# Kernel optimization log

Hardware: AMD Instinct MI355X
Metric: run time of the kernel (lower is better)

## Reference

```python
import jax, jax.numpy as jnp
import numpy as np

B, T, D, H, N = 16, 512, 256, 4, 10
DK = D // H
EPS = 1e-12  # espnet LayerNorm eps


def _pe(t, d):
    # espnet PositionalEncoding table
    pos = np.arange(t, dtype=np.float32)[:, None]
    div = np.exp(np.arange(0, d, 2, dtype=np.float32) * (-np.log(10000.0) / d))
    pe = np.zeros((t, d), dtype=np.float32)
    pe[:, 0::2] = np.sin(pos * div)
    pe[:, 1::2] = np.cos(pos * div)
    return jnp.asarray(pe)


def _ln(x, g, b):
    m = jnp.mean(x, -1, keepdims=True)
    v = jnp.var(x, -1, keepdims=True)
    return (x - m) * jax.lax.rsqrt(v + EPS) * g + b


def _forward(x, x_lengths, lids, Wq, bq, Wk, bk, Wv, bv, Wo, bo, W1, b1, W2, b2, g1, be1, g2, be2, gf, bef):
    b, t, d = x.shape
    pe = _pe(t, d)
    pad = jnp.arange(t)[None, :] < x_lengths[:, None]          # [b,t] non-pad mask
    amask = pad[:, None, None, :]                               # [b,1,1,t] key mask
    onehot = (lids[:, None] == jnp.arange(N)[None, :]).astype(x.dtype)  # [b,N]
    h0 = x * np.float32(np.sqrt(d)) + pe[None]                  # scaled input + pos-enc (shared across experts)
    neg = jnp.finfo(x.dtype).min
    out = jnp.zeros_like(x)
    for z in range(N):  # fixed small set of structurally-distinct experts
        # pre-norm self-attention block
        hn = _ln(h0, g1[z], be1[z])
        q = (hn @ Wq[z] + bq[z]).reshape(b, t, H, DK).transpose(0, 2, 1, 3)
        k_ = (hn @ Wk[z] + bk[z]).reshape(b, t, H, DK).transpose(0, 2, 1, 3)
        v_ = (hn @ Wv[z] + bv[z]).reshape(b, t, H, DK).transpose(0, 2, 1, 3)
        scores = jnp.einsum('bhqd,bhkd->bhqk', q, k_) / np.float32(np.sqrt(DK))
        attn = jax.nn.softmax(jnp.where(amask, scores, neg), axis=-1)
        attn = jnp.where(amask, attn, jnp.zeros((), x.dtype))
        ctx = jnp.einsum('bhqk,bhkd->bhqd', attn, v_).transpose(0, 2, 1, 3).reshape(b, t, d)
        h = h0 + ctx @ Wo[z] + bo[z]
        # pre-norm feed-forward block
        hn2 = _ln(h, g2[z], be2[z])
        h = h + jax.nn.relu(hn2 @ W1[z] + b1[z]) @ W2[z] + b2[z]
        # final after_norm, then one-hot masked combine (== emb_lang sum)
        out = out + onehot[:, z, None, None] * _ln(h, gf[z], bef[z])
    return out


def setup_inputs() -> dict:
    key = jax.random.key(0)
    ks = jax.random.split(key, 12)
    s = np.float32(0.02)
    FF = 4 * D
    return {
        'x': jax.random.normal(ks[0], (B, T, D), jnp.float32),
        'x_lengths': jax.random.randint(ks[1], (B,), T // 2, T + 1),
        'lids': jax.random.randint(ks[2], (B,), 0, N),
        'Wq': jax.random.normal(ks[3], (N, D, D), jnp.float32) * s,
        'bq': jnp.zeros((N, D), jnp.float32),
        'Wk': jax.random.normal(ks[4], (N, D, D), jnp.float32) * s,
        'bk': jnp.zeros((N, D), jnp.float32),
        'Wv': jax.random.normal(ks[5], (N, D, D), jnp.float32) * s,
        'bv': jnp.zeros((N, D), jnp.float32),
        'Wo': jax.random.normal(ks[6], (N, D, D), jnp.float32) * s,
        'bo': jnp.zeros((N, D), jnp.float32),
        'W1': jax.random.normal(ks[7], (N, D, FF), jnp.float32) * s,
        'b1': jnp.zeros((N, FF), jnp.float32),
        'W2': jax.random.normal(ks[8], (N, FF, D), jnp.float32) * s,
        'b2': jnp.zeros((N, D), jnp.float32),
        'g1': jnp.ones((N, D), jnp.float32),
        'be1': jnp.zeros((N, D), jnp.float32),
        'g2': jnp.ones((N, D), jnp.float32),
        'be2': jnp.zeros((N, D), jnp.float32),
        'gf': jnp.ones((N, D), jnp.float32),
        'bef': jnp.zeros((N, D), jnp.float32),
    }


def reference(x, x_lengths, lids, Wq, bq, Wk, bk, Wv, bv, Wo, bo, W1, b1, W2, b2, g1, be1, g2, be2, gf, bef):
    return _forward(x, x_lengths, lids, Wq, bq, Wk, bk, Wv, bv, Wo, bo, W1, b1, W2, b2, g1, be1, g2, be2, gf, bef)
```

## Files before the change

kernel.cpp:

```cpp
#include <hip/hip_runtime.h>

typedef unsigned short u16;
typedef __bf16 bf16x8 __attribute__((ext_vector_type(8)));
typedef float  f32x4  __attribute__((ext_vector_type(4)));
typedef unsigned int   u32x4 __attribute__((ext_vector_type(4)));
typedef unsigned short u16x4 __attribute__((ext_vector_type(4)));

#define DEV __device__ __forceinline__

#define NB   16
#define TT   512
#define DD   256
#define HH   4
#define DKH  64
#define NLANG 10
#define FFD  1024

DEV u16 f2bf(float f) {
  unsigned int u = __builtin_bit_cast(unsigned int, f);
  return (u16)((u + 0x7fffu + ((u >> 16) & 1u)) >> 16);
}

DEV f32x4 zero4() { f32x4 z; z[0]=0.f; z[1]=0.f; z[2]=0.f; z[3]=0.f; return z; }

typedef __attribute__((address_space(1))) const unsigned int g_as1;
typedef __attribute__((address_space(3))) unsigned int l_as3;
DEV void load_lds16(const void* g, void* l) {
  __builtin_amdgcn_global_load_lds((g_as1*)g, (l_as3*)l, 16, 0, 0);
}

DEV bf16x8 lds_frag(const u16* lds, int row, int slot) {
  return *(const bf16x8*)(lds + row * 64 + ((slot ^ (row & 7)) << 3));
}

__global__ __launch_bounds__(256) void pre_kernel(
    const float* __restrict__ Wq, const float* __restrict__ Wk,
    const float* __restrict__ Wv, const float* __restrict__ Wo,
    const float* __restrict__ W1, const float* __restrict__ W2,
    u16* __restrict__ wtq, u16* __restrict__ wtk, u16* __restrict__ wtv,
    u16* __restrict__ wto, u16* __restrict__ wt1, u16* __restrict__ wt2,
    const float* __restrict__ x, float* __restrict__ h0, u16* __restrict__ hn,
    const float* __restrict__ g, const float* __restrict__ be,
    const int* __restrict__ lids) {
  __shared__ u16 tile[32][33];
  const int bx = blockIdx.x;
  if (bx < 7680) {
    const float* src; u16* dst; int R, C, z, r0, c0;
    if (bx < 2560) {
      const int w = bx / 640, rem = bx % 640;
      src = (w == 0) ? Wq : (w == 1) ? Wk : (w == 2) ? Wv : Wo;
      dst = (w == 0) ? wtq : (w == 1) ? wtk : (w == 2) ? wtv : wto;
      R = 256; C = 256; z = rem >> 6;
      const int rc = rem & 63; r0 = (rc >> 3) * 32; c0 = (rc & 7) * 32;
    } else if (bx < 5120) {
      const int rem = bx - 2560; src = W1; dst = wt1; R = 256; C = 1024;
      z = rem >> 8; const int rc = rem & 255; r0 = (rc >> 5) * 32; c0 = (rc & 31) * 32;
    } else {
      const int rem = bx - 5120; src = W2; dst = wt2; R = 1024; C = 256;
      z = rem >> 8; const int rc = rem & 255; r0 = (rc >> 3) * 32; c0 = (rc & 7) * 32;
    }
    bool used = false;
#pragma unroll
    for (int i = 0; i < NB; ++i) used |= (lids[i] == z);
    if (!used) return;
    const float* s = src + (size_t)z * R * C;
    u16* d = dst + (size_t)z * R * C;
    const int tx = threadIdx.x & 31, ty = threadIdx.x >> 5;
#pragma unroll
    for (int rr = 0; rr < 4; ++rr) {
      const int r = ty + rr * 8;
      tile[r][tx] = f2bf(s[(size_t)(r0 + r) * C + c0 + tx]);
    }
    __syncthreads();
#pragma unroll
    for (int rr = 0; rr < 4; ++rr) {
      const int cc = ty + rr * 8;
      d[(size_t)(c0 + cc) * R + r0 + tx] = tile[tx][cc];
    }
  } else {
    const int wave = threadIdx.x >> 6, lane = threadIdx.x & 63;
    const int row = (bx - 7680) * 4 + wave;
    const int b = row >> 9, t = row & 511;
    const int z = lids[b];
    const int c0 = lane * 4;
    const float4 xv = *(const float4*)(x + (size_t)row * DD + c0);
    const float kPE = -9.21034037197618f / 256.0f;
    float div0 = __expf(kPE * (float)c0);
    float div1 = __expf(kPE * (float)(c0 + 2));
    float a0 = div0 * (float)t, a1 = div1 * (float)t;
    float h[4];
    h[0] = xv.x * 16.0f + sinf(a0);
    h[1] = xv.y * 16.0f + cosf(a0);
    h[2] = xv.z * 16.0f + sinf(a1);
    h[3] = xv.w * 16.0f + cosf(a1);
    float s = h[0] + h[1] + h[2] + h[3];
    float ss = h[0]*h[0] + h[1]*h[1] + h[2]*h[2] + h[3]*h[3];
#pragma unroll
    for (int d = 1; d < 64; d <<= 1) { s += __shfl_xor(s, d); ss += __shfl_xor(ss, d); }
    float mean = s * (1.0f / 256.0f);
    float var  = ss * (1.0f / 256.0f) - mean * mean;
    float rstd = rsqrtf(var + 1e-12f);
    *(float4*)(h0 + (size_t)row * DD + c0) = make_float4(h[0], h[1], h[2], h[3]);
    u16x4 o;
#pragma unroll
    for (int j = 0; j < 4; ++j)
      o[j] = f2bf((h[j] - mean) * rstd * g[z * DD + c0 + j] + be[z * DD + c0 + j]);
    *(u16x4*)(hn + (size_t)row * DD + c0) = o;
  }
}

DEV void gemm_tile(const u16* __restrict__ A, const u16* __restrict__ W, int K,
                   int m0, int n0, u16* Alds, u16* Blds, f32x4 acc[4][4]) {
  const int tid = threadIdx.x;
  const int lane = tid & 63;
  const int wave = tid >> 6;
  const int wm = wave >> 1, wn = wave & 1;
  const int l15 = lane & 15, lhi = lane >> 4;
  const int lr = lane >> 3, lsl = lane & 7;
  const u16* srcA[4]; const u16* srcB[4];
#pragma unroll
  for (int j = 0; j < 4; ++j) {
    const int r = wave * 32 + j * 8 + lr;
    srcA[j] = A + (size_t)(m0 + r) * K + ((lsl ^ (r & 7)) << 3);
    srcB[j] = W + (size_t)(n0 + r) * K + ((lsl ^ (r & 7)) << 3);
  }
  for (int k0 = 0; k0 < K; k0 += 64) {
#pragma unroll
    for (int j = 0; j < 4; ++j) {
      load_lds16(srcA[j] + k0, Alds + (wave * 32 + j * 8) * 64);
      load_lds16(srcB[j] + k0, Blds + (wave * 32 + j * 8) * 64);
    }
    __syncthreads();
#pragma unroll
    for (int ks = 0; ks < 2; ++ks) {
      const int slot = ks * 4 + lhi;
      bf16x8 af[4], bfr[4];
#pragma unroll
      for (int m = 0; m < 4; ++m)
        af[m] = lds_frag(Alds, wm * 64 + m * 16 + l15, slot);
#pragma unroll
      for (int n = 0; n < 4; ++n)
        bfr[n] = lds_frag(Blds, wn * 64 + n * 16 + l15, slot);
#pragma unroll
      for (int m = 0; m < 4; ++m)
#pragma unroll
        for (int n = 0; n < 4; ++n)
          acc[m][n] = __builtin_amdgcn_mfma_f32_16x16x32_bf16(af[m], bfr[n], acc[m][n], 0, 0, 0);
    }
    __syncthreads();
  }
}

template<int EPI>
__global__ __launch_bounds__(256) void gemm_kernel(const u16* __restrict__ A,
                                                   const u16* __restrict__ Wt,
                                                   const float* __restrict__ bias,
                                                   void* __restrict__ outp,
                                                   const int* __restrict__ lids,
                                                   int N, int K) {
  __shared__ u16 Alds[128 * 64];
  __shared__ u16 Blds[128 * 64];
  const int b = blockIdx.z;
  const int z = lids[b];
  const int m0 = blockIdx.y * 128, n0 = blockIdx.x * 128;
  f32x4 acc[4][4];
#pragma unroll
  for (int i = 0; i < 4; ++i)
#pragma unroll
    for (int j = 0; j < 4; ++j) acc[i][j] = zero4();
  gemm_tile(A + (size_t)b * TT * K, Wt + (size_t)z * N * K, K, m0, n0, Alds, Blds, acc);
  const int lane = threadIdx.x & 63, wave = threadIdx.x >> 6;
  const int wm = wave >> 1, wn = wave & 1;
  const int l15 = lane & 15, lhi = lane >> 4;
  float bvv[4];
#pragma unroll
  for (int n = 0; n < 4; ++n) bvv[n] = bias[(size_t)z * N + n0 + wn * 64 + n * 16 + l15];
#pragma unroll
  for (int m = 0; m < 4; ++m) {
    const int grow = m0 + wm * 64 + m * 16 + lhi * 4;
#pragma unroll
    for (int n = 0; n < 4; ++n) {
      const int gcol = n0 + wn * 64 + n * 16 + l15;
#pragma unroll
      for (int r = 0; r < 4; ++r) {
        float v = acc[m][n][r] + bvv[n];
        size_t idx = (size_t)b * TT * N + (size_t)(grow + r) * N + gcol;
        if (EPI == 1) ((u16*)outp)[idx] = f2bf(v > 0.f ? v : 0.f);
        else ((u16*)outp)[idx] = f2bf(v);
      }
    }
  }
}

__global__ __launch_bounds__(256) void gemm_qkv(const u16* __restrict__ A,
                                                const u16* __restrict__ wtq,
                                                const u16* __restrict__ wtk,
                                                const u16* __restrict__ wtv,
                                                const float* __restrict__ bq,
                                                const float* __restrict__ bk,
                                                const float* __restrict__ bv,
                                                u16* __restrict__ qo,
                                                u16* __restrict__ ko,
                                                u16* __restrict__ vto,
                                                const int* __restrict__ lids) {
  __shared__ u16 Alds[128 * 64];
  __shared__ u16 Blds[128 * 64];
  const int b = blockIdx.z & 15, which = blockIdx.z >> 4;
  const int z = lids[b];
  const u16* W = (which == 0) ? wtq : (which == 1) ? wtk : wtv;
  const float* bias = (which == 0) ? bq : (which == 1) ? bk : bv;
  const int m0 = blockIdx.y * 128, n0 = blockIdx.x * 128;
  f32x4 acc[4][4];
#pragma unroll
  for (int i = 0; i < 4; ++i)
#pragma unroll
    for (int j = 0; j < 4; ++j) acc[i][j] = zero4();
  gemm_tile(A + (size_t)b * TT * DD, W + (size_t)z * DD * DD, DD, m0, n0, Alds, Blds, acc);
  const int lane = threadIdx.x & 63, wave = threadIdx.x >> 6;
  const int wm = wave >> 1, wn = wave & 1;
  const int l15 = lane & 15, lhi = lane >> 4;
  float bvv[4];
#pragma unroll
  for (int n = 0; n < 4; ++n) bvv[n] = bias[(size_t)z * DD + n0 + wn * 64 + n * 16 + l15];
  if (which < 2) {
    u16* out = (which == 0) ? qo : ko;
#pragma unroll
    for (int m = 0; m < 4; ++m) {
      const int grow = m0 + wm * 64 + m * 16 + lhi * 4;
#pragma unroll
      for (int n = 0; n < 4; ++n) {
        const int gcol = n0 + wn * 64 + n * 16 + l15;
#pragma unroll
        for (int r = 0; r < 4; ++r)
          out[(size_t)b * TT * DD + (size_t)(grow + r) * DD + gcol] = f2bf(acc[m][n][r] + bvv[n]);
      }
    }
  } else {
#pragma unroll
    for (int m = 0; m < 4; ++m) {
      const int grow = m0 + wm * 64 + m * 16 + lhi * 4;
#pragma unroll
      for (int n = 0; n < 4; ++n) {
        const int gcol = n0 + wn * 64 + n * 16 + l15;
        u16x4 pk;
#pragma unroll
        for (int r = 0; r < 4; ++r) pk[r] = f2bf(acc[m][n][r] + bvv[n]);
        *(u16x4*)(vto + (size_t)(b * HH + (gcol >> 6)) * DKH * TT + (size_t)(gcol & 63) * TT + grow) = pk;
      }
    }
  }
}

__global__ __launch_bounds__(512, 4) void attn_kernel(const u16* __restrict__ q,
                                                      const u16* __restrict__ k,
                                                      const u16* __restrict__ vt,
                                                      u16* __restrict__ ctx,
                                                      const int* __restrict__ lens) {
  __shared__ char smem[33792];
  const int id = blockIdx.x;
  const int qt = id >> 6, bh = id & 63, b = bh >> 2, h = bh & 3;
  const int tid = threadIdx.x;
  const int lane = tid & 63, wave = tid >> 6;
  const int grp = wave >> 2, wq = wave & 3;
  const int l15 = lane & 15, lhi = lane >> 4;
  const int len = lens[b];
  const int nt = (len + 127) >> 7;
  const int qrow0 = qt * 64 + wq * 16;
  const u16* qb = q + (size_t)b * TT * DD + h * DKH;
  const u16* kb = k + (size_t)b * TT * DD + h * DKH;
  const u16* vtb = vt + (size_t)(b * HH + h) * DKH * TT;
  const float SC = 0.125f * 1.4426950408889634f;

  u16* Pg = (u16*)(smem + wave * 4096);
  float* Of = (float*)smem;
  float* Ml = (float*)(smem + 32768);
  float* Ll = (float*)(smem + 33024);

  bf16x8 qf[2];
#pragma unroll
  for (int ks = 0; ks < 2; ++ks)
    qf[ks] = *(const bf16x8*)(qb + (size_t)(qrow0 + l15) * DD + ks * 32 + lhi * 8);

  float m[4] = {-1e30f, -1e30f, -1e30f, -1e30f};
  float l[4] = {0.f, 0.f, 0.f, 0.f};
  f32x4 o[4];
#pragma unroll
  for (int d0 = 0; d0 < 4; ++d0) o[d0] = zero4();

  for (int t = grp; t < nt; t += 2) {
    f32x4 S[8];
#pragma unroll
    for (int nb = 0; nb < 8; ++nb) {
      f32x4 a = zero4();
#pragma unroll
      for (int ks = 0; ks < 2; ++ks) {
        bf16x8 kf = *(const bf16x8*)(kb + (size_t)(t * 128 + nb * 16 + l15) * DD + ks * 32 + lhi * 8);
        a = __builtin_amdgcn_mfma_f32_16x16x32_bf16(qf[ks], kf, a, 0, 0, 0);
      }
      S[nb] = a;
    }
    float tmax[4] = {-1e30f, -1e30f, -1e30f, -1e30f};
#pragma unroll
    for (int nb = 0; nb < 8; ++nb) {
      const int col = t * 128 + nb * 16 + l15;
#pragma unroll
      for (int r = 0; r < 4; ++r) {
        float v = S[nb][r] * SC;
        v = (col < len) ? v : -1e30f;
        S[nb][r] = v;
        tmax[r] = fmaxf(tmax[r], v);
      }
    }
#pragma unroll
    for (int d = 1; d < 16; d <<= 1)
#pragma unroll
      for (int r = 0; r < 4; ++r) tmax[r] = fmaxf(tmax[r], __shfl_xor(tmax[r], d));
    float al[4];
#pragma unroll
    for (int r = 0; r < 4; ++r) {
      float mn = fmaxf(m[r], tmax[r]);
      al[r] = exp2f(m[r] - mn);
      m[r] = mn;
    }
    float rs[4] = {0.f, 0.f, 0.f, 0.f};
#pragma unroll
    for (int nb = 0; nb < 8; ++nb) {
#pragma unroll
      for (int r = 0; r < 4; ++r) {
        float p = exp2f(S[nb][r] - m[r]);
        rs[r] += p;
        const int row16 = lhi * 4 + r;
        const int swzb = ((nb * 16 + l15) * 2) ^ ((row16 & 7) << 4);
        Pg[(row16 * 256 + swzb) >> 1] = f2bf(p);
      }
    }
#pragma unroll
    for (int d = 1; d < 16; d <<= 1)
#pragma unroll
      for (int r = 0; r < 4; ++r) rs[r] += __shfl_xor(rs[r], d);
#pragma unroll
    for (int r = 0; r < 4; ++r) l[r] = l[r] * al[r] + rs[r];
#pragma unroll
    for (int d0 = 0; d0 < 4; ++d0)
#pragma unroll
      for (int r = 0; r < 4; ++r) o[d0][r] *= al[r];
#pragma unroll
    for (int ks = 0; ks < 4; ++ks) {
      const int swz = (ks * 64 + lhi * 16) ^ ((l15 & 7) << 4);
      bf16x8 pf = *(const bf16x8*)(Pg + ((l15 * 256 + swz) >> 1));
#pragma unroll
      for (int d0 = 0; d0 < 4; ++d0) {
        bf16x8 vf = *(const bf16x8*)(vtb + (size_t)(d0 * 16 + l15) * TT + t * 128 + ks * 32 + lhi * 8);
        o[d0] = __builtin_amdgcn_mfma_f32_16x16x32_bf16(pf, vf, o[d0], 0, 0, 0);
      }
    }
  }

  __syncthreads();
  if (grp == 1) {
#pragma unroll
    for (int d0 = 0; d0 < 4; ++d0)
#pragma unroll
      for (int r = 0; r < 4; ++r)
        Of[(wq * 16 + lhi * 4 + r) * 68 + d0 * 16 + l15] = o[d0][r];
    if (l15 == 0) {
#pragma unroll
      for (int r = 0; r < 4; ++r) {
        Ml[wq * 16 + lhi * 4 + r] = m[r];
        Ll[wq * 16 + lhi * 4 + r] = l[r];
      }
    }
  }
  __syncthreads();
  if (grp == 0) {
    u16* cb = ctx + (size_t)b * TT * DD + h * DKH;
#pragma unroll
    for (int r = 0; r < 4; ++r) {
      const int lrow = wq * 16 + lhi * 4 + r;
      const float m1 = Ml[lrow], l1 = Ll[lrow];
      const float mn = fmaxf(m[r], m1);
      const float a0 = exp2f(m[r] - mn), a1 = exp2f(m1 - mn);
      const float linv = 1.0f / (l[r] * a0 + l1 * a1);
#pragma unroll
      for (int d0 = 0; d0 < 4; ++d0) {
        const float of = Of[lrow * 68 + d0 * 16 + l15];
        const float out = (o[d0][r] * a0 + of * a1) * linv;
        cb[(size_t)(qt * 64 + lrow) * DD + d0 * 16 + l15] = f2bf(out);
      }
    }
  }
}

template<int FINAL>
__global__ __launch_bounds__(512) void gemm_ln_kernel(
    const u16* __restrict__ A, const u16* __restrict__ Wt,
    const float* __restrict__ bias, const float* __restrict__ res,
    float* __restrict__ outf, u16* __restrict__ outbf,
    const float* __restrict__ g, const float* __restrict__ be,
    const int* __restrict__ lids, int K) {
  __shared__ u16 Alds[32 * 64];
  __shared__ u16 Blds[256 * 64];
  __shared__ float Sred[2][4][16];
  __shared__ float SSred[2][4][16];
  const int b = blockIdx.y;
  const int z = lids[b];
  const int m0 = blockIdx.x * 32;
  const int tid = threadIdx.x, lane = tid & 63, wave = tid >> 6;
  const int l15 = lane & 15, lhi = lane >> 4;
  const int lr = lane >> 3, lsl = lane & 7;
  const u16* Ab = A + (size_t)b * TT * K;
  const u16* Wb = Wt + (size_t)z * 256 * K;
  const u16* srcA = Ab;
  if (wave < 4) {
    const int rA = wave * 8 + lr;
    srcA = Ab + (size_t)(m0 + rA) * K + ((lsl ^ (rA & 7)) << 3);
  }
  const u16* srcB[4];
#pragma unroll
  for (int j = 0; j < 4; ++j) {
    const int rB = wave * 32 + j * 8 + lr;
    srcB[j] = Wb + (size_t)rB * K + ((lsl ^ (rB & 7)) << 3);
  }
  f32x4 acc[4];
#pragma unroll
  for (int n = 0; n < 4; ++n) acc[n] = zero4();
  for (int k0 = 0; k0 < K; k0 += 64) {
    if (wave < 4) load_lds16(srcA + k0, Alds + (wave * 8) * 64);
#pragma unroll
    for (int j = 0; j < 4; ++j)
      load_lds16(srcB[j] + k0, Blds + (wave * 32 + j * 8) * 64);
    __syncthreads();
#pragma unroll
    for (int ks = 0; ks < 2; ++ks) {
      const int slot = ks * 4 + lhi;
      bf16x8 af = lds_frag(Alds, (wave >> 2) * 16 + l15, slot);
#pragma unroll
      for (int n = 0; n < 4; ++n) {
        bf16x8 bf = lds_frag(Blds, (wave & 3) * 64 + n * 16 + l15, slot);
        acc[n] = __builtin_amdgcn_mfma_f32_16x16x32_bf16(af, bf, acc[n], 0, 0, 0);
      }
    }
    __syncthreads();
  }
  const int rbase = m0 + (wave >> 2) * 16;
  const int cq = (wave & 3) * 64;
  float bv[4], gv[4], bev[4];
#pragma unroll
  for (int n = 0; n < 4; ++n) {
    const int col = cq + n * 16 + l15;
    bv[n]  = bias[(size_t)z * 256 + col];
    gv[n]  = g[(size_t)z * 256 + col];
    bev[n] = be[(size_t)z * 256 + col];
  }
  float v[4][4];
  float sr[4] = {0.f, 0.f, 0.f, 0.f}, ssr[4] = {0.f, 0.f, 0.f, 0.f};
#pragma unroll
  for (int n = 0; n < 4; ++n) {
#pragma unroll
    for (int r = 0; r < 4; ++r) {
      const size_t idx = ((size_t)b * TT + rbase + lhi * 4 + r) * 256 + cq + n * 16 + l15;
      float t = acc[n][r] + bv[n] + res[idx];
      v[n][r] = t;
      sr[r] += t;
      ssr[r] += t * t;
    }
  }
#pragma unroll
  for (int d = 1; d < 16; d <<= 1)
#pragma unroll
    for (int r = 0; r < 4; ++r) { sr[r] += __shfl_xor(sr[r], d); ssr[r] += __shfl_xor(ssr[r], d); }
  if (l15 == 0) {
#pragma unroll
    for (int r = 0; r < 4; ++r) {
      Sred[wave >> 2][wave & 3][lhi * 4 + r] = sr[r];
      SSred[wave >> 2][wave & 3][lhi * 4 + r] = ssr[r];
    }
  }
  __syncthreads();
  float meanr[4], rstdr[4];
#pragma unroll
  for (int r = 0; r < 4; ++r) {
    float tot = 0.f, tss = 0.f;
#pragma unroll
    for (int qd = 0; qd < 4; ++qd) {
      tot += Sred[wave >> 2][qd][lhi * 4 + r];
      tss += SSred[wave >> 2][qd][lhi * 4 + r];
    }
    const float mean = tot * (1.0f / 256.0f);
    const float var  = tss * (1.0f / 256.0f) - mean * mean;
    meanr[r] = mean;
    rstdr[r] = rsqrtf(var + 1e-12f);
  }
#pragma unroll
  for (int n = 0; n < 4; ++n) {
#pragma unroll
    for (int r = 0; r < 4; ++r) {
      const size_t idx = ((size_t)b * TT + rbase + lhi * 4 + r) * 256 + cq + n * 16 + l15;
      const float ln = (v[n][r] - meanr[r]) * rstdr[r] * gv[n] + bev[n];
      if (FINAL) {
        outf[idx] = ln;
      } else {
        outf[idx] = v[n][r];
        outbf[idx] = f2bf(ln);
      }
    }
  }
}

extern "C" void kernel_launch(void* const* d_in, const int* in_sizes, int n_in,
                              void* d_out, int out_size, void* d_ws, size_t ws_size,
                              hipStream_t stream) {
  (void)in_sizes; (void)n_in; (void)out_size; (void)ws_size;
  const float* x    = (const float*)d_in[0];
  const int*   xlen = (const int*)d_in[1];
  const int*   lids = (const int*)d_in[2];
  const float* Wq = (const float*)d_in[3];
  const float* bq = (const float*)d_in[4];
  const float* Wk = (const float*)d_in[5];
  const float* bk = (const float*)d_in[6];
  const float* Wv = (const float*)d_in[7];
  const float* bv = (const float*)d_in[8];
  const float* Wo = (const float*)d_in[9];
  const float* bo = (const float*)d_in[10];
  const float* W1 = (const float*)d_in[11];
  const float* b1 = (const float*)d_in[12];
  const float* W2 = (const float*)d_in[13];
  const float* b2 = (const float*)d_in[14];
  const float* g1 = (const float*)d_in[15];
  const float* be1= (const float*)d_in[16];
  const float* g2 = (const float*)d_in[17];
  const float* be2= (const float*)d_in[18];
  const float* gf = (const float*)d_in[19];
  const float* bef= (const float*)d_in[20];

  char* ws = (char*)d_ws;
  size_t off = 0;
  auto alloc = [&](size_t bytes) -> void* {
    void* p = ws + off;
    off = (off + bytes + 255) & ~(size_t)255;
    return p;
  };
  u16* wtq = (u16*)alloc((size_t)NLANG * DD * DD * 2);
  u16* wtk = (u16*)alloc((size_t)NLANG * DD * DD * 2);
  u16* wtv = (u16*)alloc((size_t)NLANG * DD * DD * 2);
  u16* wto = (u16*)alloc((size_t)NLANG * DD * DD * 2);
  u16* wt1 = (u16*)alloc((size_t)NLANG * DD * FFD * 2);
  u16* wt2 = (u16*)alloc((size_t)NLANG * FFD * DD * 2);
  float* h0 = (float*)alloc((size_t)NB * TT * DD * 4);
  float* hc = (float*)alloc((size_t)NB * TT * DD * 4);
  u16* hn  = (u16*)alloc((size_t)NB * TT * DD * 2);
  u16* qb  = (u16*)alloc((size_t)NB * TT * DD * 2);
  u16* kb  = (u16*)alloc((size_t)NB * TT * DD * 2);
  u16* vtb = (u16*)alloc((size_t)NB * TT * DD * 2);
  u16* ctx = (u16*)alloc((size_t)NB * TT * DD * 2);
  u16* ffn = (u16*)alloc((size_t)NB * TT * FFD * 2);

  pre_kernel<<<dim3(7680 + 2048), 256, 0, stream>>>(
      Wq, Wk, Wv, Wo, W1, W2, wtq, wtk, wtv, wto, wt1, wt2,
      x, h0, hn, g1, be1, lids);

  gemm_qkv<<<dim3(2, 4, 48), 256, 0, stream>>>(hn, wtq, wtk, wtv, bq, bk, bv, qb, kb, vtb, lids);

  attn_kernel<<<dim3(512), 512, 0, stream>>>(qb, kb, vtb, ctx, xlen);

  gemm_ln_kernel<0><<<dim3(16, NB), 512, 0, stream>>>(ctx, wto, bo, h0, hc, hn, g2, be2, lids, DD);

  gemm_kernel<1><<<dim3(8, 4, NB), 256, 0, stream>>>(hn, wt1, b1, ffn, lids, FFD, DD);

  gemm_ln_kernel<1><<<dim3(16, NB), 512, 0, stream>>>(ffn, wt2, b2, hc, (float*)d_out, nullptr, gf, bef, lids, FFD);
}
```

Baseline: 105.7 us.

## Drop split-KV wave groups in attention, batch K/V loads ahead of MFMAs

The attention kernel no longer splits each 64-query tile's key range across two wave groups and merges partial softmax states through shared memory. Each block now runs 4 waves that each walk all key tiles, which removes the two __syncthreads, the LDS merge and the extra exp2. The K and V fragment loads are also hoisted into register arrays before their MFMA chains so several loads can be in flight at once. The cost is half the per-block parallelism over keys and higher register pressure from the batched fragments.

```diff
diff --git a/kernel.cpp b/kernel.cpp
--- a/kernel.cpp
+++ b/kernel.cpp
@@ -251,30 +251,26 @@
   }
 }
 
-__global__ __launch_bounds__(512, 4) void attn_kernel(const u16* __restrict__ q,
-                                                      const u16* __restrict__ k,
-                                                      const u16* __restrict__ vt,
-                                                      u16* __restrict__ ctx,
-                                                      const int* __restrict__ lens) {
-  __shared__ char smem[33792];
+__global__ void attn_kernel(const u16* __restrict__ q,
+                            const u16* __restrict__ k,
+                            const u16* __restrict__ vt,
+                            u16* __restrict__ ctx,
+                            const int* __restrict__ lens) {
+  __shared__ u16 Pbuf[4][2048];
   const int id = blockIdx.x;
   const int qt = id >> 6, bh = id & 63, b = bh >> 2, h = bh & 3;
   const int tid = threadIdx.x;
   const int lane = tid & 63, wave = tid >> 6;
-  const int grp = wave >> 2, wq = wave & 3;
   const int l15 = lane & 15, lhi = lane >> 4;
   const int len = lens[b];
   const int nt = (len + 127) >> 7;
-  const int qrow0 = qt * 64 + wq * 16;
+  const int qrow0 = qt * 64 + wave * 16;
   const u16* qb = q + (size_t)b * TT * DD + h * DKH;
   const u16* kb = k + (size_t)b * TT * DD + h * DKH;
   const u16* vtb = vt + (size_t)(b * HH + h) * DKH * TT;
   const float SC = 0.125f * 1.4426950408889634f;
 
-  u16* Pg = (u16*)(smem + wave * 4096);
-  float* Of = (float*)smem;
-  float* Ml = (float*)(smem + 32768);
-  float* Ll = (float*)(smem + 33024);
+  u16* Pg = Pbuf[wave];
 
   bf16x8 qf[2];
 #pragma unroll
@@ -287,17 +283,22 @@
 #pragma unroll
   for (int d0 = 0; d0 < 4; ++d0) o[d0] = zero4();
 
-  for (int t = grp; t < nt; t += 2) {
+  for (int t = 0; t < nt; ++t) {
     f32x4 S[8];
-#pragma unroll
-    for (int nb = 0; nb < 8; ++nb) {
-      f32x4 a = zero4();
-#pragma unroll
-      for (int ks = 0; ks < 2; ++ks) {
-        bf16x8 kf = *(const bf16x8*)(kb + (size_t)(t * 128 + nb * 16 + l15) * DD + ks * 32 + lhi * 8);
-        a = __builtin_amdgcn_mfma_f32_16x16x32_bf16(qf[ks], kf, a, 0, 0, 0);
-      }
-      S[nb] = a;
+    {
+      bf16x8 kf[8];
+#pragma unroll
+      for (int nb = 0; nb < 8; ++nb)
+        kf[nb] = *(const bf16x8*)(kb + (size_t)(t * 128 + nb * 16 + l15) * DD + lhi * 8);
+#pragma unroll
+      for (int nb = 0; nb < 8; ++nb)
+        S[nb] = __builtin_amdgcn_mfma_f32_16x16x32_bf16(qf[0], kf[nb], zero4(), 0, 0, 0);
+#pragma unroll
+      for (int nb = 0; nb < 8; ++nb)
+        kf[nb] = *(const bf16x8*)(kb + (size_t)(t * 128 + nb * 16 + l15) * DD + 32 + lhi * 8);
+#pragma unroll
+      for (int nb = 0; nb < 8; ++nb)
+        S[nb] = __builtin_amdgcn_mfma_f32_16x16x32_bf16(qf[1], kf[nb], S[nb], 0, 0, 0);
     }
     float tmax[4] = {-1e30f, -1e30f, -1e30f, -1e30f};
 #pragma unroll
@@ -348,47 +349,25 @@
     for (int ks = 0; ks < 4; ++ks) {
       const int swz = (ks * 64 + lhi * 16) ^ ((l15 & 7) << 4);
       bf16x8 pf = *(const bf16x8*)(Pg + ((l15 * 256 + swz) >> 1));
-#pragma unroll
-      for (int d0 = 0; d0 < 4; ++d0) {
-        bf16x8 vf = *(const bf16x8*)(vtb + (size_t)(d0 * 16 + l15) * TT + t * 128 + ks * 32 + lhi * 8);
-        o[d0] = __builtin_amdgcn_mfma_f32_16x16x32_bf16(pf, vf, o[d0], 0, 0, 0);
-      }
-    }
-  }
-
-  __syncthreads();
-  if (grp == 1) {
-#pragma unroll
-    for (int d0 = 0; d0 < 4; ++d0)
-#pragma unroll
-      for (int r = 0; r < 4; ++r)
-        Of[(wq * 16 + lhi * 4 + r) * 68 + d0 * 16 + l15] = o[d0][r];
-    if (l15 == 0) {
-#pragma unroll
-      for (int r = 0; r < 4; ++r) {
-        Ml[wq * 16 + lhi * 4 + r] = m[r];
-        Ll[wq * 16 + lhi * 4 + r] = l[r];
-      }
-    }
-  }
-  __syncthreads();
-  if (grp == 0) {
-    u16* cb = ctx + (size_t)b * TT * DD + h * DKH;
-#pragma unroll
-    for (int r = 0; r < 4; ++r) {
-      const int lrow = wq * 16 + lhi * 4 + r;
-      const float m1 = Ml[lrow], l1 = Ll[lrow];
-      const float mn = fmaxf(m[r], m1);
-      const float a0 = exp2f(m[r] - mn), a1 = exp2f(m1 - mn);
-      const float linv = 1.0f / (l[r] * a0 + l1 * a1);
-#pragma unroll
-      for (int d0 = 0; d0 < 4; ++d0) {
-        const float of = Of[lrow * 68 + d0 * 16 + l15];
-        const float out = (o[d0][r] * a0 + of * a1) * linv;
-        cb[(size_t)(qt * 64 + lrow) * DD + d0 * 16 + l15] = f2bf(out);
-      }
-    }
-  }
+      bf16x8 vf[4];
+#pragma unroll
+      for (int d0 = 0; d0 < 4; ++d0)
+        vf[d0] = *(const bf16x8*)(vtb + (size_t)(d0 * 16 + l15) * TT + t * 128 + ks * 32 + lhi * 8);
+#pragma unroll
+      for (int d0 = 0; d0 < 4; ++d0)
+        o[d0] = __builtin_amdgcn_mfma_f32_16x16x32_bf16(pf, vf[d0], o[d0], 0, 0, 0);
+    }
+  }
+
+  float linv[4];
+#pragma unroll
+  for (int r = 0; r < 4; ++r) linv[r] = 1.0f / l[r];
+  u16* cb = ctx + (size_t)b * TT * DD + h * DKH;
+#pragma unroll
+  for (int d0 = 0; d0 < 4; ++d0)
+#pragma unroll
+    for (int r = 0; r < 4; ++r)
+      cb[(size_t)(qrow0 + lhi * 4 + r) * DD + d0 * 16 + l15] = f2bf(o[d0][r] * linv[r]);
 }
 
 template<int FINAL>
@@ -561,7 +540,7 @@
 
   gemm_qkv<<<dim3(2, 4, 48), 256, 0, stream>>>(hn, wtq, wtk, wtv, bq, bk, bv, qb, kb, vtb, lids);
 
-  attn_kernel<<<dim3(512), 512, 0, stream>>>(qb, kb, vtb, ctx, xlen);
+  attn_kernel<<<dim3(512), 256, 0, stream>>>(qb, kb, vtb, ctx, xlen);
 
   gemm_ln_kernel<0><<<dim3(16, NB), 512, 0, stream>>>(ctx, wto, bo, h0, hc, hn, g2, be2, lids, DD);
 
```

After: 108.7 us. 2.9% more time.
